# Optimization experiments

Measured on AMD Instinct MI355X. Metric: run time of the kernel, lower is better.

The kernel has to match this reference:

```python
import jax, jax.numpy as jnp
import numpy as np

EMB = 1024
HEADS = 16
EPS = 1e-6


def setup_inputs() -> dict:
    key = jax.random.key(0)
    ks = jax.random.split(key, 11)
    B, T = 4, 2048
    s = 0.02
    inp = {
        "x": jax.random.normal(ks[0], (B, T, EMB), dtype=jnp.float32),
        "Wq": jax.random.normal(ks[1], (EMB, EMB), dtype=jnp.float32) * s,
        "bq": jnp.zeros((EMB,), dtype=jnp.float32),
        "Wk": jax.random.normal(ks[2], (EMB, EMB), dtype=jnp.float32) * s,
        "bk": jnp.zeros((EMB,), dtype=jnp.float32),
        "Wv": jax.random.normal(ks[3], (EMB, EMB), dtype=jnp.float32) * s,
        "bv": jnp.zeros((EMB,), dtype=jnp.float32),
        "Wp": jax.random.normal(ks[4], (EMB, EMB), dtype=jnp.float32) * s,
        "bp": jnp.zeros((EMB,), dtype=jnp.float32),
        "gamma": jnp.ones((EMB,), dtype=jnp.float32),
        "beta": jnp.zeros((EMB,), dtype=jnp.float32),
    }
    return inp


def reference(x, Wq, bq, Wk, bk, Wv, bv, Wp, bp, gamma, beta):
    B, T, E = x.shape
    H = HEADS
    hd = E // H
    residual = x
    # torch Linear: y = x @ W.T + b
    q = (jnp.einsum('bte,fe->btf', x, Wq) + bq).reshape(B, T, H, hd).transpose(0, 2, 1, 3)
    k = (jnp.einsum('bte,fe->btf', x, Wk) + bk).reshape(B, T, H, hd).transpose(0, 2, 1, 3)
    v = (jnp.einsum('bte,fe->btf', x, Wv) + bv).reshape(B, T, H, hd).transpose(0, 2, 1, 3)
    # NOTE: original scales by 1/sqrt(T), not 1/sqrt(head_size)
    scale = 1.0 / jnp.sqrt(jnp.asarray(T, dtype=x.dtype))
    att = jnp.einsum('bhqd,bhkd->bhqk', q, k) * scale
    causal = jnp.tril(jnp.ones((T, T), dtype=bool))
    att = jnp.where(causal, att, -jnp.inf)
    att = jax.nn.softmax(att, axis=-1)
    out = jnp.einsum('bhqk,bhkd->bhqd', att, v)
    out = out.transpose(0, 2, 1, 3).reshape(B, T, E)
    # residual added BEFORE projection (as in original)
    out = jnp.einsum('bte,fe->btf', out + residual, Wp) + bp
    # LayerNorm(eps=1e-6)
    mu = jnp.mean(out, axis=-1, keepdims=True)
    var = jnp.mean(jnp.square(out - mu), axis=-1, keepdims=True)
    out = (out - mu) / jnp.sqrt(var + EPS) * gamma + beta
    return out
```

## Files before the change

kernel.cpp:

```cpp
#include <hip/hip_runtime.h>
#include <hip/hip_bf16.h>
#include <cstdint>
#include <cstdio>

#define EMB    1024
#define HEADS  16
#define HD     64
#define TSEQ   2048
#define NBATCH 4
#define BT     (NBATCH*TSEQ)
#define QKVN   3072
#define QKLD   2048

#define CSCALE (1.4426950408889634f * 0.022097086912079608f)

typedef __hip_bfloat16 bf16;
typedef __attribute__((ext_vector_type(8))) short short8;
typedef __attribute__((ext_vector_type(4))) short short4v;
typedef __attribute__((ext_vector_type(4))) float f32x4;

__device__ __forceinline__ void gload_lds16(const void* g, void* l) {
  __builtin_amdgcn_global_load_lds(
      (const __attribute__((address_space(1))) void*)g,
      (__attribute__((address_space(3))) void*)l,
      16, 0, 0);
}

__global__ void fused_cast(const float* __restrict__ x, const float* __restrict__ Wq,
                           const float* __restrict__ Wk, const float* __restrict__ Wv,
                           const float* __restrict__ Wp, const float* __restrict__ bq,
                           const float* __restrict__ bk, const float* __restrict__ bv,
                           bf16* __restrict__ xb, bf16* __restrict__ wqkv,
                           bf16* __restrict__ wpb, float* __restrict__ biasqkv) {
  const int blk = blockIdx.x;
  const int i = threadIdx.x * 4;
  if (blk >= 12288) {
    const int wsel = blk - 12288;
    const float* bsrc = wsel == 0 ? bq : (wsel == 1 ? bk : bv);
    float4 bv4 = *(const float4*)(bsrc + i);
    if (wsel == 0) { bv4.x *= CSCALE; bv4.y *= CSCALE; bv4.z *= CSCALE; bv4.w *= CSCALE; }
    *(float4*)(biasqkv + wsel * 1024 + i) = bv4;
    return;
  }
  const float* src; bf16* dst; float sc = 1.0f;
  if (blk < 8192)       { src = x  + (size_t)blk * 1024;           dst = xb   + (size_t)blk * 1024; }
  else if (blk < 9216)  { src = Wq + (size_t)(blk - 8192) * 1024;  dst = wqkv + (size_t)(blk - 8192) * 1024; sc = CSCALE; }
  else if (blk < 10240) { src = Wk + (size_t)(blk - 9216) * 1024;  dst = wqkv + ((size_t)1 << 20) + (size_t)(blk - 9216) * 1024; }
  else if (blk < 11264) { src = Wv + (size_t)(blk - 10240) * 1024; dst = wqkv + ((size_t)2 << 20) + (size_t)(blk - 10240) * 1024; }
  else                  { src = Wp + (size_t)(blk - 11264) * 1024; dst = wpb  + (size_t)(blk - 11264) * 1024; }
  float4 v = *(const float4*)(src + i);
  union { short4v v; bf16 b[4]; } u;
  u.b[0] = __float2bfloat16(v.x * sc); u.b[1] = __float2bfloat16(v.y * sc);
  u.b[2] = __float2bfloat16(v.z * sc); u.b[3] = __float2bfloat16(v.w * sc);
  *(short4v*)(dst + i) = u.v;
}

template<int MODE>
__global__ __launch_bounds__(256) void gemm_bt(
    const bf16* __restrict__ A, const bf16* __restrict__ B,
    const float* __restrict__ bias, void* __restrict__ out0,
    bf16* __restrict__ vt, int M, int N, int K) {
  __shared__ bf16 As[128 * 32];
  __shared__ bf16 Bs[128 * 32];
  const int tid = threadIdx.x;
  const int l = tid & 63, w = tid >> 6;
  const int r = l & 15, q = l >> 4;
  const int m0 = blockIdx.y * 128, n0 = blockIdx.x * 128;
  const int wm = w >> 1, wn = w & 1;

  f32x4 acc[4][4];
#pragma unroll
  for (int i = 0; i < 4; ++i)
#pragma unroll
    for (int j = 0; j < 4; ++j) acc[i][j] = (f32x4){0.f, 0.f, 0.f, 0.f};

  const int slot0 = w * 64 + l;
  const int rowS0 = slot0 >> 2, chS0 = (slot0 & 3) * 8;
  const int slot1 = 256 + slot0;
  const int rowS1 = slot1 >> 2, chS1 = (slot1 & 3) * 8;

  const bf16* A0 = A + (size_t)(m0 + rowS0) * K + chS0;
  const bf16* A1 = A + (size_t)(m0 + rowS1) * K + chS1;
  const bf16* B0 = B + (size_t)(n0 + rowS0) * K + chS0;
  const bf16* B1 = B + (size_t)(n0 + rowS1) * K + chS1;
  char* AsD0 = (char*)As + w * 1024;
  char* AsD1 = (char*)As + 4096 + w * 1024;
  char* BsD0 = (char*)Bs + w * 1024;
  char* BsD1 = (char*)Bs + 4096 + w * 1024;

  for (int k0 = 0; k0 < K; k0 += 32) {
    __syncthreads();
    gload_lds16(A0 + k0, AsD0);
    gload_lds16(A1 + k0, AsD1);
    gload_lds16(B0 + k0, BsD0);
    gload_lds16(B1 + k0, BsD1);
    __syncthreads();

    short8 af[4], bfr[4];
#pragma unroll
    for (int mt = 0; mt < 4; ++mt)
      af[mt] = *(const short8*)(As + (wm * 64 + mt * 16 + r) * 32 + q * 8);
#pragma unroll
    for (int nt = 0; nt < 4; ++nt)
      bfr[nt] = *(const short8*)(Bs + (wn * 64 + nt * 16 + r) * 32 + q * 8);
#pragma unroll
    for (int mt = 0; mt < 4; ++mt)
#pragma unroll
      for (int nt = 0; nt < 4; ++nt)
        acc[mt][nt] = __builtin_amdgcn_mfma_f32_16x16x32_bf16(af[mt], bfr[nt], acc[mt][nt], 0, 0, 0);
  }

#pragma unroll
  for (int nt = 0; nt < 4; ++nt) {
    const int col = n0 + wn * 64 + nt * 16 + r;
    const float bv = bias[col];
#pragma unroll
    for (int mt = 0; mt < 4; ++mt) {
#pragma unroll
      for (int reg = 0; reg < 4; ++reg) {
        const int row = m0 + wm * 64 + mt * 16 + q * 4 + reg;
        const float v = acc[mt][nt][reg] + bv;
        if (MODE == 1) {
          ((float*)out0)[(size_t)row * N + col] = v;
        } else if (n0 < 2048) {
          ((bf16*)out0)[(size_t)row * QKLD + col] = __float2bfloat16(v);
        } else {
          const int f = col - 2048, h = f >> 6, d = f & 63;
          const int b = row >> 11, t = row & 2047;
          const int swz = (t & ~63) | ((((t >> 3) ^ d) & 7) << 3) | (t & 7);
          vt[((size_t)(b * 16 + h) * 64 + d) * 2048 + swz] = __float2bfloat16(v);
        }
      }
    }
  }
}

__global__ __launch_bounds__(256, 2) void flash4(
    const bf16* __restrict__ qk, const bf16* __restrict__ vt,
    const float* __restrict__ x, bf16* __restrict__ pb) {
  const int bh = blockIdx.x;
  const int ip = blockIdx.y;
  const int b = bh >> 4, h = bh & 15;
  const int qt[4] = { 31 - ip, 23 - ip, ip + 8, ip };
  const int tid = threadIdx.x, l = tid & 63, w = tid >> 6;
  const int r = l & 15, quad = l >> 4;

  __shared__ bf16 VtL[2][64 * 64];
  __shared__ bf16 Pl[2][4][16 * 72];

  const bf16* Qbase = qk + (size_t)b * TSEQ * QKLD + h * HD;
  const bf16* Kbase = Qbase + 1024;
  const bf16* Vhead = vt + (size_t)bh * 64 * 2048;

  const int sl0 = tid, sl1 = 256 + tid;
  const bf16* vg0 = Vhead + (size_t)(sl0 >> 3) * 2048 + (sl0 & 7) * 8;
  const bf16* vg1 = Vhead + (size_t)(sl1 >> 3) * 2048 + (sl1 & 7) * 8;
  char* ldsb0[2] = { (char*)&VtL[0][0] + w * 1024, (char*)&VtL[1][0] + w * 1024 };
  char* ldsb1[2] = { (char*)&VtL[0][0] + 4096 + w * 1024, (char*)&VtL[1][0] + 4096 + w * 1024 };

  short8 qf0[4], qf1[4];
#pragma unroll
  for (int t = 0; t < 4; ++t) {
    const bf16* qp = Qbase + (size_t)(qt[t] * 64 + w * 16 + r) * QKLD + quad * 8;
    qf0[t] = *(const short8*)qp;
    qf1[t] = *(const short8*)(qp + 32);
  }

  f32x4 o[4][4], lac[4];
#pragma unroll
  for (int t = 0; t < 4; ++t) {
    lac[t] = (f32x4){0.f, 0.f, 0.f, 0.f};
#pragma unroll
    for (int nt = 0; nt < 4; ++nt) o[t][nt] = (f32x4){0.f, 0.f, 0.f, 0.f};
  }

  short8 ones;
#pragma unroll
  for (int j = 0; j < 8; ++j) ones[j] = (short)0x3F80;

  short8 kf0[4], kf1[4];
  const int c0 = quad ^ (r & 7);

  auto step = [&](int t, const bf16* V, bf16* PlW, bool diag) {
    f32x4 s[4];
#pragma unroll
    for (int nt = 0; nt < 4; ++nt) {
      f32x4 a = (f32x4){0.f, 0.f, 0.f, 0.f};
      a = __builtin_amdgcn_mfma_f32_16x16x32_bf16(qf0[t], kf0[nt], a, 0, 0, 0);
      a = __builtin_amdgcn_mfma_f32_16x16x32_bf16(qf1[t], kf1[nt], a, 0, 0, 0);
      s[nt] = a;
    }
#pragma unroll
    for (int nt = 0; nt < 4; ++nt)
#pragma unroll
      for (int reg = 0; reg < 4; ++reg) {
        float v = s[nt][reg];
        if (diag) {
          const int kj = nt * 16 + r;
          const int qi = w * 16 + quad * 4 + reg;
          if (kj > qi) v = -__builtin_inff();
        }
        PlW[(quad * 4 + reg) * 72 + nt * 16 + r] = __float2bfloat16(exp2f(v));
      }
    const short8 pf0 = *(const short8*)(PlW + r * 72 + quad * 8);
    const short8 pf1 = *(const short8*)(PlW + r * 72 + 32 + quad * 8);
#pragma unroll
    for (int nt = 0; nt < 4; ++nt) {
      const int d = nt * 16 + r;
      const short8 vf0 = *(const short8*)(V + d * 64 + c0 * 8);
      const short8 vf1 = *(const short8*)(V + d * 64 + (c0 ^ 4) * 8);
      o[t][nt] = __builtin_amdgcn_mfma_f32_16x16x32_bf16(pf0, vf0, o[t][nt], 0, 0, 0);
      o[t][nt] = __builtin_amdgcn_mfma_f32_16x16x32_bf16(pf1, vf1, o[t][nt], 0, 0, 0);
    }
    lac[t] = __builtin_amdgcn_mfma_f32_16x16x32_bf16(pf0, ones, lac[t], 0, 0, 0);
    lac[t] = __builtin_amdgcn_mfma_f32_16x16x32_bf16(pf1, ones, lac[t], 0, 0, 0);
  };

  gload_lds16(vg0, ldsb0[0]);
  gload_lds16(vg1, ldsb1[0]);
  int bsel = 0;

  const int ktmax = qt[0];
  for (int kt = 0; kt <= ktmax; ++kt) {
#pragma unroll
    for (int nt = 0; nt < 4; ++nt) {
      const bf16* kp = Kbase + (size_t)(kt * 64 + nt * 16 + r) * QKLD + quad * 8;
      kf0[nt] = *(const short8*)kp;
      kf1[nt] = *(const short8*)(kp + 32);
    }
    __syncthreads();
    if (kt < ktmax) {
      gload_lds16(vg0 + (kt + 1) * 64, ldsb0[bsel ^ 1]);
      gload_lds16(vg1 + (kt + 1) * 64, ldsb1[bsel ^ 1]);
    }
    const bf16* V = &VtL[bsel][0];
    step(0, V, &Pl[0][w][0], kt == qt[0]);
    if (kt <= qt[1]) step(1, V, &Pl[1][w][0], kt == qt[1]);
    if (kt <= qt[2]) step(2, V, &Pl[0][w][0], kt == qt[2]);
    if (kt <= qt[3]) step(3, V, &Pl[1][w][0], kt == qt[3]);
    bsel ^= 1;
  }

#pragma unroll
  for (int t = 0; t < 4; ++t) {
#pragma unroll
    for (int reg = 0; reg < 4; ++reg) {
      const float inv = 1.0f / lac[t][reg];
      const int row = qt[t] * 64 + w * 16 + quad * 4 + reg;
      const float* xr = x + (size_t)(b * TSEQ + row) * EMB + h * HD;
      bf16* pr = pb + (size_t)(b * TSEQ + row) * EMB + h * HD;
#pragma unroll
      for (int nt = 0; nt < 4; ++nt) {
        const int d = nt * 16 + r;
        pr[d] = __float2bfloat16(o[t][nt][reg] * inv + xr[d]);
      }
    }
  }
}

__global__ __launch_bounds__(256) void ln_kernel(float* __restrict__ out,
                                                 const float* __restrict__ gamma,
                                                 const float* __restrict__ beta) {
  const int row = blockIdx.x;
  const int tid = threadIdx.x;
  float* p = out + (size_t)row * EMB;
  float4 v = ((const float4*)p)[tid];
  float s = v.x + v.y + v.z + v.w;
  float ss = v.x * v.x + v.y * v.y + v.z * v.z + v.w * v.w;
#pragma unroll
  for (int m = 1; m < 64; m <<= 1) {
    s += __shfl_xor(s, m, 64);
    ss += __shfl_xor(ss, m, 64);
  }
  __shared__ float red[8];
  const int w = tid >> 6, l = tid & 63;
  if (l == 0) { red[w] = s; red[4 + w] = ss; }
  __syncthreads();
  s = red[0] + red[1] + red[2] + red[3];
  ss = red[4] + red[5] + red[6] + red[7];
  const float mu = s * (1.0f / EMB);
  const float var = ss * (1.0f / EMB) - mu * mu;
  const float rs = rsqrtf(var + 1e-6f);
  const float4 g = ((const float4*)gamma)[tid];
  const float4 bb = ((const float4*)beta)[tid];
  float4 o;
  o.x = (v.x - mu) * rs * g.x + bb.x;
  o.y = (v.y - mu) * rs * g.y + bb.y;
  o.z = (v.z - mu) * rs * g.z + bb.z;
  o.w = (v.w - mu) * rs * g.w + bb.w;
  ((float4*)p)[tid] = o;
}

extern "C" void kernel_launch(void* const* d_in, const int* in_sizes, int n_in,
                              void* d_out, int out_size, void* d_ws, size_t ws_size,
                              hipStream_t stream) {
  const float* x     = (const float*)d_in[0];
  const float* Wq    = (const float*)d_in[1];
  const float* bq    = (const float*)d_in[2];
  const float* Wk    = (const float*)d_in[3];
  const float* bk    = (const float*)d_in[4];
  const float* Wv    = (const float*)d_in[5];
  const float* bv    = (const float*)d_in[6];
  const float* Wp    = (const float*)d_in[7];
  const float* bp    = (const float*)d_in[8];
  const float* gamma = (const float*)d_in[9];
  const float* beta  = (const float*)d_in[10];
  float* out = (float*)d_out;

  if (ws_size < (size_t)74 * 1024 * 1024) {
    printf("kernel_launch: ws_size %zu too small\n", ws_size);
    return;
  }
  char* ws = (char*)d_ws;
  bf16* xb    = (bf16*)ws;
  bf16* wqkv  = (bf16*)(ws + ((size_t)16 << 20));
  bf16* wpb   = (bf16*)(ws + ((size_t)22 << 20));
  float* bqkv = (float*)(ws + ((size_t)24 << 20));
  bf16* qkbuf = (bf16*)(ws + ((size_t)25 << 20));
  bf16* vtbuf = (bf16*)(ws + ((size_t)57 << 20));
  bf16* pbuf  = xb;

  fused_cast<<<12291, 256, 0, stream>>>(x, Wq, Wk, Wv, Wp, bq, bk, bv, xb, wqkv, wpb, bqkv);

  gemm_bt<0><<<dim3(24, 64), 256, 0, stream>>>(xb, wqkv, bqkv, qkbuf, vtbuf, BT, QKVN, EMB);

  flash4<<<dim3(64, 8), 256, 0, stream>>>(qkbuf, vtbuf, x, pbuf);

  gemm_bt<1><<<dim3(8, 64), 256, 0, stream>>>(pbuf, wpb, bp, out, nullptr, BT, EMB, EMB);

  ln_kernel<<<BT, 256, 0, stream>>>(out, gamma, beta);
}
```

Measured before the change: 325.1 us.

## Keep attention probabilities in registers via transposed S=K·Qᵀ MFMA layout

The flash kernel now computes the score tile as K times Q transposed, so each lane's accumulator output already matches the A-operand layout of 16x16x16 MFMAs. The probabilities can then be packed to bf16 in registers and fed straight into the PV and row-sum MFMAs, which removes the LDS round trip through the P buffer and its extra shared memory. V fragments are loaded once per key tile and reused across all four query tiles, and the diagonal mask is specialised at compile time. The kernel also uses a raw exp2 intrinsic and a fast bf16 pack with only approximate rounding, and it now issues twice as many smaller MFMAs for PV while holding more V fragments in registers.

```diff
diff --git a/kernel.cpp b/kernel.cpp
--- a/kernel.cpp
+++ b/kernel.cpp
@@ -19,11 +19,32 @@
 typedef __attribute__((ext_vector_type(4))) short short4v;
 typedef __attribute__((ext_vector_type(4))) float f32x4;
 
+#define MFMA32(A,B,C) __builtin_amdgcn_mfma_f32_16x16x32_bf16(A,B,C,0,0,0)
+#if __has_builtin(__builtin_amdgcn_mfma_f32_16x16x16_bf16)
+#define MFMA16(A,B,C) __builtin_amdgcn_mfma_f32_16x16x16_bf16(A,B,C,0,0,0)
+#else
+#define MFMA16(A,B,C) __builtin_amdgcn_mfma_f32_16x16x16bf16_1k(A,B,C,0,0,0)
+#endif
+
+#if __has_builtin(__builtin_amdgcn_exp2f)
+#define EXP2(x) __builtin_amdgcn_exp2f(x)
+#else
+#define EXP2(x) exp2f(x)
+#endif
+
+template<bool B> struct BoolC { static constexpr bool value = B; };
+
 __device__ __forceinline__ void gload_lds16(const void* g, void* l) {
   __builtin_amdgcn_global_load_lds(
       (const __attribute__((address_space(1))) void*)g,
       (__attribute__((address_space(3))) void*)l,
       16, 0, 0);
+}
+
+__device__ __forceinline__ unsigned pkbf(float a, float b) {
+  unsigned ua = __builtin_bit_cast(unsigned, a) + 0x8000u;
+  unsigned ub = __builtin_bit_cast(unsigned, b) + 0x8000u;
+  return __builtin_amdgcn_perm(ub, ua, 0x07060302u);
 }
 
 __global__ void fused_cast(const float* __restrict__ x, const float* __restrict__ Wq,
@@ -107,7 +128,7 @@
     for (int mt = 0; mt < 4; ++mt)
 #pragma unroll
       for (int nt = 0; nt < 4; ++nt)
-        acc[mt][nt] = __builtin_amdgcn_mfma_f32_16x16x32_bf16(af[mt], bfr[nt], acc[mt][nt], 0, 0, 0);
+        acc[mt][nt] = MFMA32(af[mt], bfr[nt], acc[mt][nt]);
   }
 
 #pragma unroll
@@ -135,7 +156,7 @@
   }
 }
 
-__global__ __launch_bounds__(256, 2) void flash4(
+__global__ __launch_bounds__(256, 2) void flash5(
     const bf16* __restrict__ qk, const bf16* __restrict__ vt,
     const float* __restrict__ x, bf16* __restrict__ pb) {
   const int bh = blockIdx.x;
@@ -146,7 +167,6 @@
   const int r = l & 15, quad = l >> 4;
 
   __shared__ bf16 VtL[2][64 * 64];
-  __shared__ bf16 Pl[2][4][16 * 72];
 
   const bf16* Qbase = qk + (size_t)b * TSEQ * QKLD + h * HD;
   const bf16* Kbase = Qbase + 1024;
@@ -174,70 +194,83 @@
     for (int nt = 0; nt < 4; ++nt) o[t][nt] = (f32x4){0.f, 0.f, 0.f, 0.f};
   }
 
-  short8 ones;
-#pragma unroll
-  for (int j = 0; j < 8; ++j) ones[j] = (short)0x3F80;
+  short4v ones4;
+#pragma unroll
+  for (int j = 0; j < 4; ++j) ones4[j] = (short)0x3F80;
 
   short8 kf0[4], kf1[4];
-  const int c0 = quad ^ (r & 7);
-
-  auto step = [&](int t, const bf16* V, bf16* PlW, bool diag) {
-    f32x4 s[4];
-#pragma unroll
-    for (int nt = 0; nt < 4; ++nt) {
-      f32x4 a = (f32x4){0.f, 0.f, 0.f, 0.f};
-      a = __builtin_amdgcn_mfma_f32_16x16x32_bf16(qf0[t], kf0[nt], a, 0, 0, 0);
-      a = __builtin_amdgcn_mfma_f32_16x16x32_bf16(qf1[t], kf1[nt], a, 0, 0, 0);
-      s[nt] = a;
-    }
-#pragma unroll
-    for (int nt = 0; nt < 4; ++nt)
-#pragma unroll
-      for (int reg = 0; reg < 4; ++reg) {
-        float v = s[nt][reg];
-        if (diag) {
-          const int kj = nt * 16 + r;
-          const int qi = w * 16 + quad * 4 + reg;
-          if (kj > qi) v = -__builtin_inff();
-        }
-        PlW[(quad * 4 + reg) * 72 + nt * 16 + r] = __float2bfloat16(exp2f(v));
-      }
-    const short8 pf0 = *(const short8*)(PlW + r * 72 + quad * 8);
-    const short8 pf1 = *(const short8*)(PlW + r * 72 + 32 + quad * 8);
-#pragma unroll
-    for (int nt = 0; nt < 4; ++nt) {
-      const int d = nt * 16 + r;
-      const short8 vf0 = *(const short8*)(V + d * 64 + c0 * 8);
-      const short8 vf1 = *(const short8*)(V + d * 64 + (c0 ^ 4) * 8);
-      o[t][nt] = __builtin_amdgcn_mfma_f32_16x16x32_bf16(pf0, vf0, o[t][nt], 0, 0, 0);
-      o[t][nt] = __builtin_amdgcn_mfma_f32_16x16x32_bf16(pf1, vf1, o[t][nt], 0, 0, 0);
-    }
-    lac[t] = __builtin_amdgcn_mfma_f32_16x16x32_bf16(pf0, ones, lac[t], 0, 0, 0);
-    lac[t] = __builtin_amdgcn_mfma_f32_16x16x32_bf16(pf1, ones, lac[t], 0, 0, 0);
-  };
+  short4v vf[4][4];
 
   gload_lds16(vg0, ldsb0[0]);
   gload_lds16(vg1, ldsb1[0]);
   int bsel = 0;
 
   const int ktmax = qt[0];
+  const int qrow_l = w * 16 + r;
   for (int kt = 0; kt <= ktmax; ++kt) {
 #pragma unroll
-    for (int nt = 0; nt < 4; ++nt) {
-      const bf16* kp = Kbase + (size_t)(kt * 64 + nt * 16 + r) * QKLD + quad * 8;
-      kf0[nt] = *(const short8*)kp;
-      kf1[nt] = *(const short8*)(kp + 32);
+    for (int g = 0; g < 4; ++g) {
+      const bf16* kp = Kbase + (size_t)(kt * 64 + g * 16 + r) * QKLD + quad * 8;
+      kf0[g] = *(const short8*)kp;
+      kf1[g] = *(const short8*)(kp + 32);
     }
     __syncthreads();
     if (kt < ktmax) {
       gload_lds16(vg0 + (kt + 1) * 64, ldsb0[bsel ^ 1]);
       gload_lds16(vg1 + (kt + 1) * 64, ldsb1[bsel ^ 1]);
     }
-    const bf16* V = &VtL[bsel][0];
-    step(0, V, &Pl[0][w][0], kt == qt[0]);
-    if (kt <= qt[1]) step(1, V, &Pl[1][w][0], kt == qt[1]);
-    if (kt <= qt[2]) step(2, V, &Pl[0][w][0], kt == qt[2]);
-    if (kt <= qt[3]) step(3, V, &Pl[1][w][0], kt == qt[3]);
+    {
+      const bf16* V = &VtL[bsel][0];
+#pragma unroll
+      for (int nt = 0; nt < 4; ++nt)
+#pragma unroll
+        for (int g = 0; g < 4; ++g)
+          vf[nt][g] = *(const short4v*)(V + (nt * 16 + r) * 64 +
+                                        (((g * 2 + (quad >> 1)) ^ (r & 7)) * 8) + (quad & 1) * 4);
+    }
+
+    auto tilestep = [&](int t, auto diagc) {
+      constexpr bool D = decltype(diagc)::value;
+      f32x4 s[4];
+#pragma unroll
+      for (int g = 0; g < 4; ++g) {
+        f32x4 a = (f32x4){0.f, 0.f, 0.f, 0.f};
+        a = MFMA32(kf0[g], qf0[t], a);
+        a = MFMA32(kf1[g], qf1[t], a);
+        s[g] = a;
+      }
+      short4v pA[4];
+#pragma unroll
+      for (int g = 0; g < 4; ++g) {
+        float p[4];
+#pragma unroll
+        for (int reg = 0; reg < 4; ++reg) {
+          float e = EXP2(s[g][reg]);
+          if (D) {
+            const int kj = g * 16 + quad * 4 + reg;
+            if (kj > qrow_l) e = 0.f;
+          }
+          p[reg] = e;
+        }
+        union { short4v v; unsigned u[2]; } pu;
+        pu.u[0] = pkbf(p[0], p[1]);
+        pu.u[1] = pkbf(p[2], p[3]);
+        pA[g] = pu.v;
+      }
+#pragma unroll
+      for (int nt = 0; nt < 4; ++nt)
+#pragma unroll
+        for (int g = 0; g < 4; ++g)
+          o[t][nt] = MFMA16(pA[g], vf[nt][g], o[t][nt]);
+#pragma unroll
+      for (int g = 0; g < 4; ++g)
+        lac[t] = MFMA16(pA[g], ones4, lac[t]);
+    };
+
+    if (kt == qt[0]) tilestep(0, BoolC<true>{}); else tilestep(0, BoolC<false>{});
+    if (kt <= qt[1]) { if (kt == qt[1]) tilestep(1, BoolC<true>{}); else tilestep(1, BoolC<false>{}); }
+    if (kt <= qt[2]) { if (kt == qt[2]) tilestep(2, BoolC<true>{}); else tilestep(2, BoolC<false>{}); }
+    if (kt <= qt[3]) { if (kt == qt[3]) tilestep(3, BoolC<true>{}); else tilestep(3, BoolC<false>{}); }
     bsel ^= 1;
   }
 
@@ -324,7 +357,7 @@
 
   gemm_bt<0><<<dim3(24, 64), 256, 0, stream>>>(xb, wqkv, bqkv, qkbuf, vtbuf, BT, QKVN, EMB);
 
-  flash4<<<dim3(64, 8), 256, 0, stream>>>(qkbuf, vtbuf, x, pbuf);
+  flash5<<<dim3(64, 8), 256, 0, stream>>>(qkbuf, vtbuf, x, pbuf);
 
   gemm_bt<1><<<dim3(8, 64), 256, 0, stream>>>(pbuf, wpb, bp, out, nullptr, BT, EMB, EMB);
 
```

New measurement: 308.8 us. 1.05x faster.
